# Optimization experiments

Hardware: AMD Instinct MI355X
Metric: run time of the kernel (lower is better)

Reference implementation:

```python
import jax, jax.numpy as jnp
import numpy as np


def _wn_dense_relu(x, v, g, bias):
    # torch weight_norm over dim=0: w[h,:] = g[h] * v[h,:] / ||v[h,:]||
    w = g[:, None] * v / jnp.linalg.norm(v, axis=1, keepdims=True)  # (hid, inp)
    return jax.nn.relu(jnp.einsum('bld,hd->blh', x, w) + bias)


def _masked_softmax(scores, mask, axis):
    # additive large-negative masking, numerically stable softmax
    return jax.nn.softmax(scores + jnp.where(mask > 0, 0.0, -1e9), axis=axis)


def setup_inputs() -> dict:
    key = jax.random.key(0)
    ks = jax.random.split(key, 6)
    B, La, Lb, D, H = 8, 2048, 2048, 256, 256
    return {
        'a': jax.random.normal(ks[0], (B, La, D), dtype=jnp.float32),
        'b': jax.random.normal(ks[1], (B, Lb, D), dtype=jnp.float32),
        'mask_a': jax.random.randint(ks[2], (B, La), 0, 2, dtype=jnp.int32),
        'mask_b': jax.random.randint(ks[3], (B, Lb), 0, 2, dtype=jnp.int32),
        'a_v': jax.random.normal(ks[4], (H, D), dtype=jnp.float32) * (2.0 / D) ** 0.5,
        'a_g': jnp.ones((H,), dtype=jnp.float32),
        'a_bias': jnp.zeros((H,), dtype=jnp.float32),
        'b_v': jax.random.normal(ks[5], (H, D), dtype=jnp.float32) * (2.0 / D) ** 0.5,
        'b_g': jnp.ones((H,), dtype=jnp.float32),
        'b_bias': jnp.zeros((H,), dtype=jnp.float32),
        'tau': jnp.asarray((1.0 / H) ** 0.5, dtype=jnp.float32),
    }


def reference(a, b, mask_a, mask_b, a_v, a_g, a_bias, b_v, b_g, b_bias, tau):
    ha = _wn_dense_relu(a, a_v, a_g, a_bias)                 # (B, La, H)
    hb = _wn_dense_relu(b, b_v, b_g, b_bias)                 # (B, Lb, H)
    attn = jnp.einsum('bih,bjh->bij', ha, hb) * tau          # (B, La, Lb)
    weight_a = _masked_softmax(attn, mask_a[:, :, None], axis=1)  # softmax over La
    weight_b = _masked_softmax(attn, mask_b[:, None, :], axis=2)  # softmax over Lb
    align_a = jnp.einsum('bij,bjd->bid', weight_b, b)        # (B, La, D)
    align_b = jnp.einsum('bij,bid->bjd', weight_a, a)        # (B, Lb, D)
    return align_a, align_b
```

## Files before the change

### kernel.cpp

```cpp
#include <hip/hip_runtime.h>
#include <hip/hip_bf16.h>
#include <stdint.h>

#define B_   8
#define L_   2048
#define D_   256
#define H_   256
#define TJ   64
#define NT   (L_/TJ)
#define BM   128
#define LOG2E 1.4426950408889634f

typedef short bf16x8 __attribute__((ext_vector_type(8)));
typedef short bf16x4 __attribute__((ext_vector_type(4)));
typedef float f32x4  __attribute__((ext_vector_type(4)));

#define MFMA(a,b,c) __builtin_amdgcn_mfma_f32_16x16x32_bf16(a,b,c,0,0,0)
#define EX2(x) __builtin_amdgcn_exp2f(x)

typedef unsigned int u32;
__device__ __forceinline__ void gload_lds16(const void* g, void* l){
  __builtin_amdgcn_global_load_lds((const __attribute__((address_space(1))) u32*)g,
                                   (__attribute__((address_space(3))) u32*)l, 16, 0, 0);
}

__device__ __forceinline__ unsigned short f2bf(float f){
  __hip_bfloat16 h = __float2bfloat16(f);
  unsigned short us;
  __builtin_memcpy(&us, &h, 2);
  return us;
}

__device__ __forceinline__ void bar_lgkm(){
  asm volatile("s_waitcnt lgkmcnt(0)" ::: "memory");
  __builtin_amdgcn_s_barrier();
  __builtin_amdgcn_sched_barrier(0);
}
__device__ __forceinline__ void bar_all(){
  asm volatile("s_waitcnt vmcnt(0) lgkmcnt(0)" ::: "memory");
  __builtin_amdgcn_s_barrier();
  __builtin_amdgcn_sched_barrier(0);
}

__global__ __launch_bounds__(256) void wnorm_kernel(const float* __restrict__ av,
      const float* __restrict__ ag, const float* __restrict__ bv,
      const float* __restrict__ bg, unsigned short* __restrict__ wa,
      unsigned short* __restrict__ wb, float* __restrict__ maxn){
  int sel = blockIdx.y;
  if (blockIdx.x == 0 && threadIdx.x < 8) maxn[sel*8 + threadIdx.x] = 0.f;
  const float* v = sel ? bv : av;
  const float* g = sel ? bg : ag;
  unsigned short* w = sel ? wb : wa;
  int h = blockIdx.x;
  int d = threadIdx.x;
  float x = v[h*D_ + d];
  float sq = x*x;
  for (int off = 32; off; off >>= 1) sq += __shfl_down(sq, off, 64);
  __shared__ float red[4];
  int lane = threadIdx.x & 63, wid = threadIdx.x >> 6;
  if (lane == 0) red[wid] = sq;
  __syncthreads();
  float tot = red[0] + red[1] + red[2] + red[3];
  float scale = g[h] / sqrtf(tot);
  w[h*D_ + d] = f2bf(x * scale);
}

__global__ __launch_bounds__(256) void hgemm_kernel(const float* __restrict__ a,
      const float* __restrict__ b, const unsigned short* __restrict__ wa,
      const unsigned short* __restrict__ wb, const float* __restrict__ a_bias,
      const float* __restrict__ b_bias, const float* __restrict__ tau_ptr,
      unsigned short* __restrict__ ha, unsigned short* __restrict__ hb,
      unsigned short* __restrict__ aT, unsigned short* __restrict__ bT,
      float* __restrict__ rn_a, float* __restrict__ rn_b,
      float* __restrict__ maxn){
  __shared__ __align__(16) unsigned short xlk[64][256];
  __shared__ float redm[4];
  int sel = blockIdx.y;
  const float* x = sel ? b : a;
  const unsigned short* w = sel ? wb : wa;
  const float* bias = sel ? b_bias : a_bias;
  unsigned short* hx = sel ? hb : ha;
  unsigned short* xT = sel ? bT : aT;
  float* rn = sel ? rn_b : rn_a;
  float scale = sel ? 1.0f : tau_ptr[0] * LOG2E;
  int m0 = blockIdx.x * 64;
  int bz = m0 / L_, l0 = m0 % L_;
  int tid = threadIdx.x;
  int lane = tid & 63, wid = tid >> 6;
  int p = lane & 15, q = lane >> 4;

  {
    int r0 = tid >> 6;
    int c  = (tid & 63) * 4;
    int slot = c >> 3, half = (c >> 2) & 1;
    #pragma unroll
    for (int it = 0; it < 16; ++it){
      int row = it*4 + r0;
      f32x4 v = *(const f32x4*)(x + (size_t)(m0 + row) * 256 + c);
      uint2 wv;
      wv.x = (u32)f2bf(v[0]) | ((u32)f2bf(v[1]) << 16);
      wv.y = (u32)f2bf(v[2]) | ((u32)f2bf(v[3]) << 16);
      *(uint2*)((char*)&xlk[row][0] + ((slot ^ (row & 7)) << 4) + half*8) = wv;
    }
  }
  __syncthreads();

  bf16x8 af[8];
  {
    int row = wid*16 + p;
    #pragma unroll
    for (int kk = 0; kk < 8; ++kk)
      af[kk] = *(const bf16x8*)((char*)&xlk[row][0] + (((kk*4 + q) ^ (row & 7)) << 4));
  }
  f32x4 acc[16] = {};
  #pragma unroll
  for (int kk = 0; kk < 8; kk++){
    #pragma unroll
    for (int n = 0; n < 16; n++){
      bf16x8 bfr = *(const bf16x8*)(w + (size_t)(n*16 + p) * 256 + kk*32 + q*8);
      acc[n] = MFMA(af[kk], bfr, acc[n]);
    }
  }

  float rs[4] = {0.f, 0.f, 0.f, 0.f};
  #pragma unroll
  for (int n = 0; n < 16; n++){
    float bv = bias[n*16 + p];
    #pragma unroll
    for (int r = 0; r < 4; r++){
      int orow = m0 + wid*16 + q*4 + r;
      float vv = acc[n][r] + bv;
      vv = vv > 0.f ? vv : 0.f;
      float sv = vv * scale;
      rs[r] += sv * sv;
      hx[(size_t)orow * 256 + n*16 + p] = f2bf(sv);
    }
  }
  #pragma unroll
  for (int off = 1; off < 16; off <<= 1)
    #pragma unroll
    for (int r = 0; r < 4; r++)
      rs[r] += __shfl_xor(rs[r], off, 64);
  float lmax = 0.f;
  float rv[4];
  #pragma unroll
  for (int r = 0; r < 4; r++){
    rv[r] = sqrtf(rs[r]) * 1.01f;
    lmax = fmaxf(lmax, rv[r]);
  }
  if (p == 0){
    #pragma unroll
    for (int r = 0; r < 4; r++)
      rn[m0 + wid*16 + q*4 + r] = rv[r];
  }
  lmax = fmaxf(lmax, __shfl_xor(lmax, 16, 64));
  lmax = fmaxf(lmax, __shfl_xor(lmax, 32, 64));
  if (lane == 0) redm[wid] = lmax;
  __syncthreads();
  if (tid == 0){
    float bm = fmaxf(fmaxf(redm[0], redm[1]), fmaxf(redm[2], redm[3]));
    atomicMax((u32*)&maxn[sel*8 + bz], __float_as_uint(bm));
  }

  #pragma unroll
  for (int it = 0; it < 16; it++){
    int d = it*16 + (tid >> 4);
    int c = (tid & 15) * 4;
    bf16x4 v;
    #pragma unroll
    for (int j = 0; j < 4; j++){
      int row = c + j;
      v[j] = (short)*((const unsigned short*)((char*)&xlk[row][0]
                + (((d >> 3) ^ (row & 7)) << 4)) + (d & 7));
    }
    *(bf16x4*)(xT + ((size_t)bz*D_ + d)*L_ + l0 + c) = v;
  }
}

__global__ __launch_bounds__(512, 2) void flash_kernel(
    const unsigned short* __restrict__ ha, const unsigned short* __restrict__ hb,
    const unsigned short* __restrict__ aT, const unsigned short* __restrict__ bT,
    const int* __restrict__ mask_a, const int* __restrict__ mask_b,
    const float* __restrict__ rn_a, const float* __restrict__ rn_b,
    const float* __restrict__ maxn, float* __restrict__ out)
{
  __shared__ __align__(16) unsigned short HBT[2][64][256];
  __shared__ __align__(16) unsigned short VTL[2][256][64];
  __shared__ __align__(16) unsigned short WT[4][32][64];
  __shared__ float SST[8][32];
  __shared__ float MSKL[2048];

  const int bid = blockIdx.x;
  const int s   = bid & 15;
  const int dir = s >> 3;
  const int bz  = s & 7;
  const int i0  = (bid >> 4) * BM;
  const int tid = threadIdx.x;
  const int lane = tid & 63;
  const int wid  = tid >> 6;
  const int wr = wid >> 1, wc = wid & 1;
  const int p = lane & 15, q = lane >> 4;

  const unsigned short* hA = dir ? hb : ha;
  const unsigned short* hB = dir ? ha : hb;
  const unsigned short* vT = dir ? aT : bT;
  const int* mask = dir ? mask_a : mask_b;
  const float* rnA = dir ? rn_b : rn_a;
  const float mxB  = maxn[(dir ^ 1)*8 + bz];
  float* outp = out + ((size_t)dir * B_ + bz) * L_ * D_;

  const unsigned short* hAp = hA + (size_t)bz * L_ * H_;
  const unsigned short* hBp = hB + (size_t)bz * L_ * H_;
  const unsigned short* vTp = vT + (size_t)bz * D_ * L_;
  const int* mp = mask + bz * L_;

  const int hb_r0 = wid*2 + (lane >> 5);
  const int hb_s  = lane & 31;
  const int vt_r0 = wid*8 + (lane >> 3);
  const int vt_s  = lane & 7;

  bf16x8 af[2][8];
  #pragma unroll
  for (int g = 0; g < 2; ++g)
    #pragma unroll
    for (int kk = 0; kk < 8; ++kk)
      af[g][kk] = *(const bf16x8*)(hAp + (size_t)(i0 + wr*32 + g*16 + p) * H_ + kk*32 + q*8);

  float m_p[2];
  #pragma unroll
  for (int g = 0; g < 2; ++g)
    m_p[g] = rnA[bz*L_ + i0 + wr*32 + g*16 + p] * mxB;

  #pragma unroll
  for (int i = 0; i < 4; ++i){
    int idx = tid + i*512;
    MSKL[idx] = (mp[idx] > 0) ? 0.f : -1e9f;
  }

  f32x4 acc[2][8];
  #pragma unroll
  for (int g = 0; g < 2; ++g)
    #pragma unroll
    for (int n = 0; n < 8; ++n) acc[g][n] = (f32x4){0.f,0.f,0.f,0.f};
  float s_run[2];
  s_run[0] = s_run[1] = 0.f;

  #define STAGE(bb, jj0) do {                                                     \
    _Pragma("unroll")                                                             \
    for (int k = 0; k < 4; ++k){                                                  \
      int rr = k*16 + hb_r0;                                                      \
      int sp = hb_s ^ (rr & 7);                                                   \
      gload_lds16(hBp + (size_t)((jj0) + rr) * H_ + sp*8,                         \
                  &HBT[bb][0][0] + (k*8192 + wid*1024)/2);                        \
    }                                                                             \
    _Pragma("unroll")                                                             \
    for (int k = 0; k < 4; ++k){                                                  \
      int rr = k*64 + vt_r0;                                                      \
      int sp = vt_s ^ (rr & 7);                                                   \
      gload_lds16(vTp + (size_t)rr * L_ + (jj0) + sp*8,                           \
                  &VTL[bb][0][0] + (k*8192 + wid*1024)/2);                        \
    }                                                                             \
  } while(0)

  STAGE(0, 0);
  bar_all();

  for (int jt = 0; jt < NT; ++jt){
    const int j0 = jt * TJ;
    const int cur = jt & 1;
    if (jt + 1 < NT) STAGE(cur ^ 1, j0 + TJ);

    f32x4 accp[2][2];
    #pragma unroll
    for (int g = 0; g < 2; ++g)
      #pragma unroll
      for (int cg = 0; cg < 2; ++cg) accp[g][cg] = (f32x4){0.f,0.f,0.f,0.f};
    __builtin_amdgcn_s_setprio(1);
    #pragma unroll
    for (int kk = 0; kk < 8; ++kk){
      const int rb = wc*32 + p;
      const int sp = ((kk*4 + q) ^ (p & 7)) * 8;
      bf16x8 b0 = *(const bf16x8*)(&HBT[cur][0][0] + rb*256 + sp);
      bf16x8 b1 = *(const bf16x8*)(&HBT[cur][0][0] + (rb+16)*256 + sp);
      accp[0][0] = MFMA(b0, af[0][kk], accp[0][0]);
      accp[1][0] = MFMA(b0, af[1][kk], accp[1][0]);
      accp[0][1] = MFMA(b1, af[0][kk], accp[0][1]);
      accp[1][1] = MFMA(b1, af[1][kk], accp[1][1]);
    }
    __builtin_amdgcn_s_setprio(0);

    f32x4 mm0 = *(const f32x4*)(&MSKL[j0 + wc*32 + q*4]);
    f32x4 mm1 = *(const f32x4*)(&MSKL[j0 + wc*32 + 16 + q*4]);

    #pragma unroll
    for (int g = 0; g < 2; ++g){
      #pragma unroll
      for (int cg = 0; cg < 2; ++cg){
        const f32x4 mm = cg ? mm1 : mm0;
        float w0 = EX2(accp[g][cg][0] + mm[0] - m_p[g]);
        float w1 = EX2(accp[g][cg][1] + mm[1] - m_p[g]);
        float w2 = EX2(accp[g][cg][2] + mm[2] - m_p[g]);
        float w3 = EX2(accp[g][cg][3] + mm[3] - m_p[g]);
        s_run[g] += (w0 + w1) + (w2 + w3);
        uint2 wv;
        wv.x = (u32)f2bf(w0) | ((u32)f2bf(w1) << 16);
        wv.y = (u32)f2bf(w2) | ((u32)f2bf(w3) << 16);
        int row = g*16 + p;
        int sl  = (wc*4 + cg*2 + (q>>1)) ^ (row & 7);
        *(uint2*)(&WT[wr][0][0] + row*64 + (sl<<3) + ((q&1)<<2)) = wv;
      }
    }
    bar_lgkm();

    bf16x8 wf[2][2];
    #pragma unroll
    for (int g = 0; g < 2; ++g)
      #pragma unroll
      for (int ks = 0; ks < 2; ++ks){
        int row = g*16 + p;
        wf[g][ks] = *(const bf16x8*)(&WT[wr][0][0] + row*64
                                     + ((((ks*4 + q) ^ (row & 7)))<<3));
      }

    __builtin_amdgcn_s_setprio(1);
    #pragma unroll
    for (int n = 0; n < 8; ++n){
      const int d = wc*128 + n*16 + p;
      #pragma unroll
      for (int ks = 0; ks < 2; ++ks){
        const int sp = ((ks*4 + q) ^ (d & 7)) * 8;
        bf16x8 vf = *(const bf16x8*)(&VTL[cur][0][0] + d*64 + sp);
        acc[0][n] = MFMA(wf[0][ks], vf, acc[0][n]);
        acc[1][n] = MFMA(wf[1][ks], vf, acc[1][n]);
      }
    }
    __builtin_amdgcn_s_setprio(0);

    bar_all();
  }
  #undef STAGE

  s_run[0] += __shfl_xor(s_run[0], 16, 64);
  s_run[0] += __shfl_xor(s_run[0], 32, 64);
  s_run[1] += __shfl_xor(s_run[1], 16, 64);
  s_run[1] += __shfl_xor(s_run[1], 32, 64);
  if (q == 0){
    SST[wid][p]      = s_run[0];
    SST[wid][16 + p] = s_run[1];
  }
  __syncthreads();
  float invS[2][4];
  #pragma unroll
  for (int g = 0; g < 2; ++g)
    #pragma unroll
    for (int r = 0; r < 4; ++r){
      int idx = g*16 + q*4 + r;
      invS[g][r] = 1.0f / (SST[wr*2][idx] + SST[wr*2 + 1][idx]);
    }

  #pragma unroll
  for (int g = 0; g < 2; ++g)
    #pragma unroll
    for (int n = 0; n < 8; ++n)
      #pragma unroll
      for (int r = 0; r < 4; ++r){
        int row = i0 + wr*32 + g*16 + q*4 + r;
        outp[(size_t)row * D_ + wc*128 + n*16 + p] = acc[g][n][r] * invS[g][r];
      }
}

extern "C" void kernel_launch(void* const* d_in, const int* in_sizes, int n_in,
                              void* d_out, int out_size, void* d_ws, size_t ws_size,
                              hipStream_t stream) {
  const float* a      = (const float*)d_in[0];
  const float* b      = (const float*)d_in[1];
  const int*   mask_a = (const int*)d_in[2];
  const int*   mask_b = (const int*)d_in[3];
  const float* a_v    = (const float*)d_in[4];
  const float* a_g    = (const float*)d_in[5];
  const float* a_bias = (const float*)d_in[6];
  const float* b_v    = (const float*)d_in[7];
  const float* b_g    = (const float*)d_in[8];
  const float* b_bias = (const float*)d_in[9];
  const float* tau    = (const float*)d_in[10];

  float* out = (float*)d_out;

  char* ws = (char*)d_ws;
  const size_t SZ_W  = (size_t)H_ * D_ * 2;
  const size_t SZ_H  = (size_t)B_ * L_ * H_ * 2;
  unsigned short* wa = (unsigned short*)(ws);
  unsigned short* wb = (unsigned short*)(ws + SZ_W);
  unsigned short* ha = (unsigned short*)(ws + 2*SZ_W);
  unsigned short* hb = (unsigned short*)(ws + 2*SZ_W + SZ_H);
  unsigned short* aT = (unsigned short*)(ws + 2*SZ_W + 2*SZ_H);
  unsigned short* bT = (unsigned short*)(ws + 2*SZ_W + 3*SZ_H);
  float* rn_a = (float*)(ws + 2*SZ_W + 4*SZ_H);
  float* rn_b = rn_a + (size_t)B_ * L_;
  float* maxn = rn_b + (size_t)B_ * L_;
  size_t need = 2*SZ_W + 4*SZ_H + 2*(size_t)B_*L_*4 + 64;
  if (ws_size < need) return;

  wnorm_kernel<<<dim3(H_, 2), 256, 0, stream>>>(a_v, a_g, b_v, b_g, wa, wb, maxn);

  {
    dim3 g((B_*L_)/64, 2);
    hgemm_kernel<<<g, 256, 0, stream>>>(a, b, wa, wb, a_bias, b_bias, tau,
                                        ha, hb, aT, bT, rn_a, rn_b, maxn);
  }

  {
    flash_kernel<<<dim3((L_/BM) * B_ * 2), 512, 0, stream>>>(
        ha, hb, aT, bT, mask_a, mask_b, rn_a, rn_b, maxn, out);
  }
}
```

Baseline: 135.3 us.

## Halve flash block tile, single-buffer LDS with staggered HB/VT staging

Cuts the flash kernel's row tile from 128 to 64 and its threads per block from 512 to 256. It drops the LDS double buffering and instead loads the next HB tile after the softmax barrier and the next VT tile after the PV barrier. The mask is stored as bf16 to save LDS. The smaller LDS footprint and doubled grid aim to raise occupancy and spread work across more CUs, at the cost of an extra barrier per iteration, less overlap between loads and compute, and twice as many re-reads of the HB and VT tiles from global memory.

Result: no change. 133.1 us (-1.6%).

```diff
diff --git a/kernel.cpp b/kernel.cpp
--- a/kernel.cpp
+++ b/kernel.cpp
@@ -8,11 +8,12 @@
 #define H_   256
 #define TJ   64
 #define NT   (L_/TJ)
-#define BM   128
+#define BM   64
 #define LOG2E 1.4426950408889634f
 
 typedef short bf16x8 __attribute__((ext_vector_type(8)));
 typedef short bf16x4 __attribute__((ext_vector_type(4)));
+typedef unsigned short u16x4 __attribute__((ext_vector_type(4)));
 typedef float f32x4  __attribute__((ext_vector_type(4)));
 
 #define MFMA(a,b,c) __builtin_amdgcn_mfma_f32_16x16x32_bf16(a,b,c,0,0,0)
@@ -29,6 +30,12 @@
   unsigned short us;
   __builtin_memcpy(&us, &h, 2);
   return us;
+}
+__device__ __forceinline__ float bf2f(unsigned short u){
+  u32 t = ((u32)u) << 16;
+  float f;
+  __builtin_memcpy(&f, &t, 4);
+  return f;
 }
 
 __device__ __forceinline__ void bar_lgkm(){
@@ -177,18 +184,18 @@
   }
 }
 
-__global__ __launch_bounds__(512, 2) void flash_kernel(
+__global__ __launch_bounds__(256, 2) void flash_kernel(
     const unsigned short* __restrict__ ha, const unsigned short* __restrict__ hb,
     const unsigned short* __restrict__ aT, const unsigned short* __restrict__ bT,
     const int* __restrict__ mask_a, const int* __restrict__ mask_b,
     const float* __restrict__ rn_a, const float* __restrict__ rn_b,
     const float* __restrict__ maxn, float* __restrict__ out)
 {
-  __shared__ __align__(16) unsigned short HBT[2][64][256];
-  __shared__ __align__(16) unsigned short VTL[2][256][64];
-  __shared__ __align__(16) unsigned short WT[4][32][64];
-  __shared__ float SST[8][32];
-  __shared__ float MSKL[2048];
+  __shared__ __align__(16) unsigned short HBT[64][256];
+  __shared__ __align__(16) unsigned short VTL[256][64];
+  __shared__ __align__(16) unsigned short WT[2][32][64];
+  __shared__ unsigned short MSKB[2048];
+  __shared__ float SST[4][32];
 
   const int bid = blockIdx.x;
   const int s   = bid & 15;
@@ -214,10 +221,10 @@
   const unsigned short* vTp = vT + (size_t)bz * D_ * L_;
   const int* mp = mask + bz * L_;
 
-  const int hb_r0 = wid*2 + (lane >> 5);
-  const int hb_s  = lane & 31;
-  const int vt_r0 = wid*8 + (lane >> 3);
-  const int vt_s  = lane & 7;
+  const int hb_r0 = tid >> 5;
+  const int hb_s  = tid & 31;
+  const int vt_r0 = tid >> 3;
+  const int vt_s  = tid & 7;
 
   bf16x8 af[2][8];
   #pragma unroll
@@ -232,9 +239,9 @@
     m_p[g] = rnA[bz*L_ + i0 + wr*32 + g*16 + p] * mxB;
 
   #pragma unroll
-  for (int i = 0; i < 4; ++i){
-    int idx = tid + i*512;
-    MSKL[idx] = (mp[idx] > 0) ? 0.f : -1e9f;
+  for (int i = 0; i < 8; ++i){
+    int idx = tid + i*256;
+    MSKB[idx] = f2bf((mp[idx] > 0) ? 0.f : -1e9f);
   }
 
   f32x4 acc[2][8];
@@ -245,30 +252,31 @@
   float s_run[2];
   s_run[0] = s_run[1] = 0.f;
 
-  #define STAGE(bb, jj0) do {                                                     \
+  #define STAGE_HB(jj0) do {                                                      \
     _Pragma("unroll")                                                             \
-    for (int k = 0; k < 4; ++k){                                                  \
-      int rr = k*16 + hb_r0;                                                      \
+    for (int k = 0; k < 8; ++k){                                                  \
+      int rr = k*8 + hb_r0;                                                       \
       int sp = hb_s ^ (rr & 7);                                                   \
       gload_lds16(hBp + (size_t)((jj0) + rr) * H_ + sp*8,                         \
-                  &HBT[bb][0][0] + (k*8192 + wid*1024)/2);                        \
+                  &HBT[0][0] + k*2048 + tid*8);                                   \
     }                                                                             \
+  } while(0)
+  #define STAGE_VT(jj0) do {                                                      \
     _Pragma("unroll")                                                             \
-    for (int k = 0; k < 4; ++k){                                                  \
-      int rr = k*64 + vt_r0;                                                      \
+    for (int k = 0; k < 8; ++k){                                                  \
+      int rr = k*32 + vt_r0;                                                      \
       int sp = vt_s ^ (rr & 7);                                                   \
       gload_lds16(vTp + (size_t)rr * L_ + (jj0) + sp*8,                           \
-                  &VTL[bb][0][0] + (k*8192 + wid*1024)/2);                        \
+                  &VTL[0][0] + k*2048 + tid*8);                                   \
     }                                                                             \
   } while(0)
 
-  STAGE(0, 0);
+  STAGE_HB(0);
+  STAGE_VT(0);
   bar_all();
 
   for (int jt = 0; jt < NT; ++jt){
     const int j0 = jt * TJ;
-    const int cur = jt & 1;
-    if (jt + 1 < NT) STAGE(cur ^ 1, j0 + TJ);
 
     f32x4 accp[2][2];
     #pragma unroll
@@ -280,8 +288,8 @@
     for (int kk = 0; kk < 8; ++kk){
       const int rb = wc*32 + p;
       const int sp = ((kk*4 + q) ^ (p & 7)) * 8;
-      bf16x8 b0 = *(const bf16x8*)(&HBT[cur][0][0] + rb*256 + sp);
-      bf16x8 b1 = *(const bf16x8*)(&HBT[cur][0][0] + (rb+16)*256 + sp);
+      bf16x8 b0 = *(const bf16x8*)(&HBT[0][0] + rb*256 + sp);
+      bf16x8 b1 = *(const bf16x8*)(&HBT[0][0] + (rb+16)*256 + sp);
       accp[0][0] = MFMA(b0, af[0][kk], accp[0][0]);
       accp[1][0] = MFMA(b0, af[1][kk], accp[1][0]);
       accp[0][1] = MFMA(b1, af[0][kk], accp[0][1]);
@@ -289,8 +297,11 @@
     }
     __builtin_amdgcn_s_setprio(0);
 
-    f32x4 mm0 = *(const f32x4*)(&MSKL[j0 + wc*32 + q*4]);
-    f32x4 mm1 = *(const f32x4*)(&MSKL[j0 + wc*32 + 16 + q*4]);
+    u16x4 k0 = *(const u16x4*)(&MSKB[j0 + wc*32 + q*4]);
+    u16x4 k1 = *(const u16x4*)(&MSKB[j0 + wc*32 + 16 + q*4]);
+    f32x4 mm0, mm1;
+    #pragma unroll
+    for (int r = 0; r < 4; ++r){ mm0[r] = bf2f(k0[r]); mm1[r] = bf2f(k1[r]); }
 
     #pragma unroll
     for (int g = 0; g < 2; ++g){
@@ -312,6 +323,8 @@
     }
     bar_lgkm();
 
+    if (jt + 1 < NT) STAGE_HB(j0 + TJ);
+
     bf16x8 wf[2][2];
     #pragma unroll
     for (int g = 0; g < 2; ++g)
@@ -329,7 +342,7 @@
       #pragma unroll
       for (int ks = 0; ks < 2; ++ks){
         const int sp = ((ks*4 + q) ^ (d & 7)) * 8;
-        bf16x8 vf = *(const bf16x8*)(&VTL[cur][0][0] + d*64 + sp);
+        bf16x8 vf = *(const bf16x8*)(&VTL[0][0] + d*64 + sp);
         acc[0][n] = MFMA(wf[0][ks], vf, acc[0][n]);
         acc[1][n] = MFMA(wf[1][ks], vf, acc[1][n]);
       }
@@ -337,8 +350,13 @@
     __builtin_amdgcn_s_setprio(0);
 
     bar_all();
-  }
-  #undef STAGE
+    if (jt + 1 < NT){
+      STAGE_VT(j0 + TJ);
+      bar_all();
+    }
+  }
+  #undef STAGE_HB
+  #undef STAGE_VT
 
   s_run[0] += __shfl_xor(s_run[0], 16, 64);
   s_run[0] += __shfl_xor(s_run[0], 32, 64);
@@ -410,7 +428,7 @@
   }
 
   {
-    flash_kernel<<<dim3((L_/BM) * B_ * 2), 512, 0, stream>>>(
+    flash_kernel<<<dim3((L_/BM) * B_ * 2), 256, 0, stream>>>(
         ha, hb, aT, bT, mask_a, mask_b, rn_a, rn_b, maxn, out);
   }
 }
```
